# Optimization experiments

Measured on AMD Instinct MI355X. Metric: run time of the kernel, lower is better.

Reference implementation:

```python
import jax, jax.numpy as jnp
import numpy as np

B, L, H, NH, DH = 2, 4096, 768, 12, 64
W_ = 128          # one-sided sliding window
NL = 2            # encoder layers
VOCAB, OUT, FF = 50265, 384, 3072
EPS = 1e-5


def _ln(x, s, b):
    m = jnp.mean(x, axis=-1, keepdims=True)
    v = jnp.mean((x - m) ** 2, axis=-1, keepdims=True)
    return (x - m) / jnp.sqrt(v + EPS) * s + b


def _attn(x, amask, Wq, bq, Wk, bk, Wv, bv, Wo, bo):
    # x: [B,L,H]; sliding-window attention (one-sided W_) + global token 0
    def heads(Wt, bt):
        return (x @ Wt + bt).reshape(B, L, NH, DH).transpose(0, 2, 1, 3)  # [B,NH,L,DH]
    q, k, v = heads(Wq, bq), heads(Wk, bk), heads(Wv, bv)
    scale = 1.0 / np.sqrt(DH).astype(np.float32)
    C = W_
    nC = L // C
    qc = q.reshape(B, NH, nC, C, DH)

    def blocks(t):  # gather [prev, self, next] key chunks -> [B,NH,nC,3C,DH]
        tc = t.reshape(B, NH, nC, C, DH)
        tp = jnp.pad(tc, ((0, 0), (0, 0), (1, 1), (0, 0), (0, 0)))
        return jnp.concatenate([tp[:, :, :-2], tp[:, :, 1:-1], tp[:, :, 2:]], axis=3)

    k3, v3 = blocks(k), blocks(v)
    s_loc = jnp.einsum('bhncd,bhnkd->bhnck', qc, k3) * scale  # [B,NH,nC,C,3C]

    pos_k = (jnp.arange(nC)[:, None] - 1) * C + jnp.arange(3 * C)[None, :]  # [nC,3C]
    pos_q = jnp.arange(nC)[:, None] * C + jnp.arange(C)[None, :]            # [nC,C]
    within = jnp.abs(pos_q[:, :, None] - pos_k[:, None, :]) <= W_           # [nC,C,3C]
    valid = (pos_k >= 0) & (pos_k < L) & (pos_k != 0)  # key 0 handled as global column
    mk = amask[:, jnp.clip(pos_k, 0, L - 1)] > 0        # [B,nC,3C]
    m = within[None, None] & valid[None, None, :, None, :] & mk[:, None, :, None, :]
    s_loc = jnp.where(m, s_loc, -1e9)

    # every token also attends to the global token 0
    s_g = jnp.einsum('bhld,bhd->bhl', q, k[:, :, 0]) * scale  # [B,NH,L]
    s = jnp.concatenate([s_loc.reshape(B, NH, L, 3 * C), s_g[..., None]], axis=-1)
    p = jax.nn.softmax(s, axis=-1)
    p_loc = p[..., :3 * C].reshape(B, NH, nC, C, 3 * C)
    out = jnp.einsum('bhnck,bhnkd->bhncd', p_loc, v3).reshape(B, NH, L, DH)
    out = out + p[..., -1:] * v[:, :, 0][:, :, None, :]

    # global token 0 attends to everything
    s0 = jnp.einsum('bhd,bhld->bhl', q[:, :, 0], k) * scale
    s0 = jnp.where(amask[:, None, :] > 0, s0, -1e9)
    o0 = jnp.einsum('bhl,bhld->bhd', jax.nn.softmax(s0, axis=-1), v)
    out = out.at[:, :, 0, :].set(o0)

    out = out.transpose(0, 2, 1, 3).reshape(B, L, H)
    return out @ Wo + bo


def setup_inputs() -> dict:
    key = jax.random.key(0)
    ks = jax.random.split(key, 16)
    p = lambda k_, sh: 0.02 * jax.random.normal(k_, sh, jnp.float32)
    return {
        'input_ids': jax.random.randint(ks[0], (B, L), 0, VOCAB, dtype=jnp.int32),
        'attention_mask': jnp.ones((B, L), jnp.int32),
        'word_emb': p(ks[1], (VOCAB, H)),
        'pos_emb': p(ks[2], (L, H)),
        'emb_ln_s': jnp.ones((H,), jnp.float32), 'emb_ln_b': jnp.zeros((H,), jnp.float32),
        'Wq': p(ks[3], (NL, H, H)), 'bq': jnp.zeros((NL, H), jnp.float32),
        'Wk': p(ks[4], (NL, H, H)), 'bk': jnp.zeros((NL, H), jnp.float32),
        'Wv': p(ks[5], (NL, H, H)), 'bv': jnp.zeros((NL, H), jnp.float32),
        'Wo': p(ks[6], (NL, H, H)), 'bo': jnp.zeros((NL, H), jnp.float32),
        'ln1_s': jnp.ones((NL, H), jnp.float32), 'ln1_b': jnp.zeros((NL, H), jnp.float32),
        'W1': p(ks[7], (NL, H, FF)), 'b1': jnp.zeros((NL, FF), jnp.float32),
        'W2': p(ks[8], (NL, FF, H)), 'b2': jnp.zeros((NL, H), jnp.float32),
        'ln2_s': jnp.ones((NL, H), jnp.float32), 'ln2_b': jnp.zeros((NL, H), jnp.float32),
        'Wfc': p(ks[9], (H, OUT)), 'bfc': jnp.zeros((OUT,), jnp.float32),
    }


def reference(input_ids, attention_mask, word_emb, pos_emb, emb_ln_s, emb_ln_b,
              Wq, bq, Wk, bk, Wv, bv, Wo, bo, ln1_s, ln1_b,
              W1, b1, W2, b2, ln2_s, ln2_b, Wfc, bfc):
    x = word_emb[input_ids] + pos_emb[None]
    x = _ln(x, emb_ln_s, emb_ln_b)
    for l in range(NL):
        a = _attn(x, attention_mask, Wq[l], bq[l], Wk[l], bk[l], Wv[l], bv[l], Wo[l], bo[l])
        x = _ln(x + a, ln1_s[l], ln1_b[l])
        h = jax.nn.gelu(x @ W1[l] + b1[l])
        x = _ln(x + h @ W2[l] + b2[l], ln2_s[l], ln2_b[l])
    v_dn = x @ Wfc + bfc           # [B,L,OUT]
    cls = v_dn[:, 0]               # fc(last_hidden[:,0]) == v_dn[:,0]
    return v_dn, cls
```

## Files before the change

kernel.cpp:

```cpp
#include <hip/hip_runtime.h>
#include <hip/hip_bf16.h>
#include <stdint.h>

#define L_SEQ 4096
#define H_DIM 768
#define N_HEADS 12
#define D_HEAD 64
#define N_CHUNK 32
#define CHUNK 128
#define FF_DIM 3072
#define OUT_DIM 384
#define BATCH 2
#define EPS_LN 1e-5f
#define M_ROWS (BATCH * L_SEQ)
#define QKV_LD (3 * H_DIM)
#define NSEG 16

typedef unsigned short u16;
typedef __bf16 bx8 __attribute__((ext_vector_type(8)));
typedef float fx4 __attribute__((ext_vector_type(4)));
typedef u16 ux8 __attribute__((ext_vector_type(8)));

__device__ __forceinline__ u16 f2bf(float f) {
  union { float f; unsigned u; } x; x.f = f;
  unsigned r = x.u + 0x7fffu + ((x.u >> 16) & 1u);
  return (u16)(r >> 16);
}
__device__ __forceinline__ float bf2f(u16 v) {
  union { unsigned u; float f; } x; x.u = ((unsigned)v) << 16;
  return x.f;
}

__device__ __forceinline__ void gload16(const void* g, void* l) {
  __builtin_amdgcn_global_load_lds((const __attribute__((address_space(1))) void*)g,
                                   (__attribute__((address_space(3))) void*)l, 16, 0, 0);
}

template<int OUT_BF16, int DO_GELU>
__global__ __launch_bounds__(256, 3)
void gemm_s(const u16* __restrict__ A, const u16* __restrict__ Bt,
            const float* __restrict__ bias,
            float* __restrict__ Cf, u16* __restrict__ Cb,
            int N, int K)
{
  __shared__ __align__(16) u16 As[128 * 64];
  __shared__ __align__(16) u16 Bs[128 * 64];
  const int tid = threadIdx.x;
  const int lane = tid & 63, w = tid >> 6;
  const int c16 = lane & 15, g = lane >> 4;
  const int wr = w >> 1, wc = w & 1;

  const int nbn = N >> 7;
  int id = blockIdx.x;
  id = (id & 7) * (gridDim.x >> 3) + (id >> 3);
  const int bm = id / nbn, bn = id % nbn;

  const int srow = w * 8 + (lane >> 3);
  const int schunk = (lane & 7) ^ (lane >> 3);
  const u16* sA = A + (size_t)(bm * 128 + srow) * K + schunk * 8;
  const u16* sB = Bt + (size_t)(bn * 128 + srow) * K + schunk * 8;
  const int wdst = w * 512;

  fx4 acc[4][4] = {};

  for (int k0 = 0; k0 < K; k0 += 64) {
    #pragma unroll
    for (int i = 0; i < 4; i++) {
      gload16(sA + (size_t)(i * 32) * K + k0, &As[i * 2048 + wdst]);
      gload16(sB + (size_t)(i * 32) * K + k0, &Bs[i * 2048 + wdst]);
    }
    __syncthreads();
    #pragma unroll
    for (int h = 0; h < 2; h++) {
      bx8 af[4], bf[4];
      #pragma unroll
      for (int m = 0; m < 4; m++) {
        const int row = wr * 64 + m * 16 + c16;
        af[m] = *(const bx8*)&As[row * 64 + (((h << 2) + g) ^ (c16 & 7)) * 8];
      }
      #pragma unroll
      for (int n = 0; n < 4; n++) {
        const int row = wc * 64 + n * 16 + c16;
        bf[n] = *(const bx8*)&Bs[row * 64 + (((h << 2) + g) ^ (c16 & 7)) * 8];
      }
      #pragma unroll
      for (int m = 0; m < 4; m++)
        #pragma unroll
        for (int n = 0; n < 4; n++)
          acc[m][n] = __builtin_amdgcn_mfma_f32_16x16x32_bf16(af[m], bf[n], acc[m][n], 0, 0, 0);
    }
    __syncthreads();
  }

  const int row0 = bm * 128 + wr * 64 + g * 4;
  const int col0 = bn * 128 + wc * 64 + c16;
  #pragma unroll
  for (int n = 0; n < 4; n++) {
    const int col = col0 + n * 16;
    const float bb = bias[col];
    #pragma unroll
    for (int m = 0; m < 4; m++) {
      #pragma unroll
      for (int r = 0; r < 4; r++) {
        float y = acc[m][n][r] + bb;
        if (DO_GELU) {
          const float tt = y;
          y = 0.5f * tt * (1.0f + tanhf(0.7978845608f * (tt + 0.044715f * tt * tt * tt)));
        }
        const size_t idx = (size_t)(row0 + m * 16 + r) * N + col;
        if (OUT_BF16) Cb[idx] = f2bf(y);
        else Cf[idx] = y;
      }
    }
  }
}

#define V_STR 424

__global__ __launch_bounds__(512, 2)
void attn_local_kernel(const u16* __restrict__ qkv, const int* __restrict__ amask,
                       u16* __restrict__ attnout)
{
  __shared__ __align__(16) u16 Vlds[64 * V_STR];
  __shared__ __align__(16) u16 Plds[8 * 16 * V_STR];

  const int tid = threadIdx.x;
  const int lane = tid & 63, w = tid >> 6;
  const int c16 = lane & 15, g = lane >> 4;

  const int bh = blockIdx.x >> 5;
  const int n = blockIdx.x & 31;
  const int b = bh / N_HEADS, h = bh % N_HEADS;

  const u16* qkvb = qkv + (size_t)b * L_SEQ * QKV_LD + h * D_HEAD;
  const int chunk_lo = n * CHUNK - CHUNK;

  for (int idx = tid; idx < 416 * 8; idx += 512) {
    const int j = idx >> 3, d8 = (idx & 7) * 8;
    if (j >= 385) {
      #pragma unroll
      for (int i = 0; i < 8; i++) Vlds[(d8 + i) * V_STR + j] = 0;
    } else {
      int pos = (j == 384) ? 0 : chunk_lo + j;
      if (pos < 0 || pos >= L_SEQ) pos = 0;
      ux8 vv = *(const ux8*)(qkvb + (size_t)pos * QKV_LD + 2 * H_DIM + d8);
      #pragma unroll
      for (int i = 0; i < 8; i++) Vlds[(d8 + i) * V_STR + j] = vv[i];
    }
  }

  const int qrow = n * CHUNK + w * 16 + c16;
  const u16* qp = qkvb + (size_t)qrow * QKV_LD + g * 8;
  const bx8 aq0 = *(const bx8*)qp;
  const bx8 aq1 = *(const bx8*)(qp + 32);

  unsigned kvm = 0;
  #pragma unroll
  for (int kf = 0; kf < 24; kf++) {
    const int pos = chunk_lo + kf * 16 + c16;
    bool ok = (pos >= 1) && (pos < L_SEQ);
    if (ok) ok = (amask[b * L_SEQ + pos] > 0);
    kvm |= ((unsigned)ok) << kf;
  }

  fx4 s[26];
  #pragma unroll
  for (int kf = 0; kf < 25; kf++) {
    int pos = (kf == 24) ? 0 : chunk_lo + kf * 16 + c16;
    if (pos < 0 || pos >= L_SEQ) pos = 0;
    const u16* kp = qkvb + (size_t)pos * QKV_LD + H_DIM + g * 8;
    const bx8 b0 = *(const bx8*)kp;
    const bx8 b1 = *(const bx8*)(kp + 32);
    fx4 a = {};
    a = __builtin_amdgcn_mfma_f32_16x16x32_bf16(aq0, b0, a, 0, 0, 0);
    a = __builtin_amdgcn_mfma_f32_16x16x32_bf16(aq1, b1, a, 0, 0, 0);
    s[kf] = a;
  }

  const int cq = w * 16 + g * 4;
  float mx[4], sm[4];
  #pragma unroll
  for (int r = 0; r < 4; r++) mx[r] = -3.0e38f;
  #pragma unroll
  for (int kf = 0; kf < 25; kf++) {
    const int j = kf * 16 + c16;
    const bool kv = (kf < 24) ? (((kvm >> kf) & 1u) != 0) : (c16 == 0);
    #pragma unroll
    for (int r = 0; r < 4; r++) {
      const int c = cq + r;
      const bool keep = kv && (kf == 24 || (j >= c && j <= c + 256));
      const float val = keep ? s[kf][r] * 0.125f : -1.0e9f;
      s[kf][r] = val;
      mx[r] = fmaxf(mx[r], val);
    }
  }
  #pragma unroll
  for (int r = 0; r < 4; r++) {
    float m = mx[r];
    m = fmaxf(m, __shfl_xor(m, 1));
    m = fmaxf(m, __shfl_xor(m, 2));
    m = fmaxf(m, __shfl_xor(m, 4));
    m = fmaxf(m, __shfl_xor(m, 8));
    mx[r] = m;
    sm[r] = 0.f;
  }
  #pragma unroll
  for (int kf = 0; kf < 25; kf++)
    #pragma unroll
    for (int r = 0; r < 4; r++) {
      const float p = __expf(s[kf][r] - mx[r]);
      s[kf][r] = p;
      sm[r] += p;
    }
  float rinv[4];
  #pragma unroll
  for (int r = 0; r < 4; r++) {
    float t = sm[r];
    t += __shfl_xor(t, 1);
    t += __shfl_xor(t, 2);
    t += __shfl_xor(t, 4);
    t += __shfl_xor(t, 8);
    rinv[r] = 1.0f / t;
  }
  s[25] = (fx4){0.f, 0.f, 0.f, 0.f};

  u16* pb = Plds + (size_t)w * 16 * V_STR;
  #pragma unroll
  for (int kf = 0; kf < 26; kf++) {
    const int j = kf * 16 + c16;
    #pragma unroll
    for (int r = 0; r < 4; r++)
      pb[(g * 4 + r) * V_STR + j] = f2bf(s[kf][r]);
  }
  __syncthreads();

  fx4 o[4] = {};
  const u16* pr = Plds + (size_t)(w * 16 + c16) * V_STR + g * 8;
  #pragma unroll
  for (int kt = 0; kt < 13; kt++) {
    const bx8 pa = *(const bx8*)(pr + kt * 32);
    #pragma unroll
    for (int df = 0; df < 4; df++) {
      const bx8 vvf = *(const bx8*)&Vlds[(df * 16 + c16) * V_STR + kt * 32 + g * 8];
      o[df] = __builtin_amdgcn_mfma_f32_16x16x32_bf16(pa, vvf, o[df], 0, 0, 0);
    }
  }

  u16* ob = attnout + (size_t)b * L_SEQ * H_DIM + h * D_HEAD;
  const int posq = n * CHUNK + w * 16 + g * 4;
  #pragma unroll
  for (int df = 0; df < 4; df++)
    #pragma unroll
    for (int r = 0; r < 4; r++)
      ob[(size_t)(posq + r) * H_DIM + df * 16 + c16] = f2bf(o[df][r] * rinv[r]);
}

__global__ __launch_bounds__(256)
void attn_g_score(const u16* __restrict__ qkv, const int* __restrict__ amask,
                  float* __restrict__ sbuf, float* __restrict__ pmax)
{
  __shared__ float qs[D_HEAD];
  __shared__ float red[4];
  const int seg = blockIdx.x, bh = blockIdx.y;
  const int b = bh / N_HEADS, h = bh % N_HEADS;
  const u16* base = qkv + (size_t)b * L_SEQ * QKV_LD + h * D_HEAD;
  const int tid = threadIdx.x;

  if (tid < D_HEAD) qs[tid] = bf2f(base[tid]);
  __syncthreads();

  const int l = seg * 256 + tid;
  const ux8* kp = (const ux8*)(base + (size_t)l * QKV_LD + H_DIM);
  float dot = 0.f;
  #pragma unroll
  for (int i = 0; i < 8; i++) {
    const ux8 kv = kp[i];
    #pragma unroll
    for (int j = 0; j < 8; j++) dot += qs[i * 8 + j] * bf2f(kv[j]);
  }
  float sv = dot * 0.125f;
  if (amask[b * L_SEQ + l] == 0) sv = -1.0e9f;
  sbuf[(size_t)bh * L_SEQ + l] = sv;

  float m = sv;
  #pragma unroll
  for (int off = 32; off > 0; off >>= 1) m = fmaxf(m, __shfl_xor(m, off));
  if ((tid & 63) == 0) red[tid >> 6] = m;
  __syncthreads();
  if (tid == 0)
    pmax[bh * NSEG + seg] = fmaxf(fmaxf(red[0], red[1]), fmaxf(red[2], red[3]));
}

__global__ __launch_bounds__(256)
void attn_g_pv(const u16* __restrict__ qkv, const float* __restrict__ sbuf,
               const float* __restrict__ pmax, float* __restrict__ psum,
               float* __restrict__ po)
{
  __shared__ float es[256];
  __shared__ float red[4];
  const int seg = blockIdx.x, bh = blockIdx.y;
  const int b = bh / N_HEADS, h = bh % N_HEADS;
  const int tid = threadIdx.x;

  float M = -3.0e38f;
  #pragma unroll
  for (int i = 0; i < NSEG; i++) M = fmaxf(M, pmax[bh * NSEG + i]);

  const int l = seg * 256 + tid;
  const float e = __expf(sbuf[(size_t)bh * L_SEQ + l] - M);
  es[tid] = e;

  float t = e;
  #pragma unroll
  for (int off = 32; off > 0; off >>= 1) t += __shfl_xor(t, off);
  if ((tid & 63) == 0) red[tid >> 6] = t;
  __syncthreads();
  if (tid == 0) psum[bh * NSEG + seg] = red[0] + red[1] + red[2] + red[3];

  const int d = tid & 63, grp = tid >> 6;
  const u16* vb = qkv + (size_t)b * L_SEQ * QKV_LD + h * D_HEAD + 2 * H_DIM + d;
  float acc = 0.f;
  #pragma unroll 4
  for (int i = 0; i < 64; i++) {
    const int ll = seg * 256 + grp * 64 + i;
    acc += es[grp * 64 + i] * bf2f(vb[(size_t)ll * QKV_LD]);
  }
  po[(((size_t)bh * NSEG + seg) * 4 + grp) * D_HEAD + d] = acc;
}

__global__ __launch_bounds__(64)
void attn_g_combine(const float* __restrict__ psum, const float* __restrict__ po,
                    u16* __restrict__ attnout)
{
  const int bh = blockIdx.x;
  const int b = bh / N_HEADS, h = bh % N_HEADS;
  const int d = threadIdx.x;
  float S = 0.f;
  #pragma unroll
  for (int i = 0; i < NSEG; i++) S += psum[bh * NSEG + i];
  float acc = 0.f;
  #pragma unroll
  for (int i = 0; i < NSEG * 4; i++)
    acc += po[((size_t)bh * NSEG * 4 + i) * D_HEAD + d];
  attnout[(size_t)b * L_SEQ * H_DIM + h * D_HEAD + d] = f2bf(acc / S);
}

__device__ __forceinline__ void block_stats(float sum, float sq, float* red,
                                            float& mean, float& rstd)
{
  const int lane = threadIdx.x & 63, wv = threadIdx.x >> 6;
  #pragma unroll
  for (int off = 32; off > 0; off >>= 1) {
    sum += __shfl_xor(sum, off);
    sq  += __shfl_xor(sq, off);
  }
  if (lane == 0) { red[wv] = sum; red[4 + wv] = sq; }
  __syncthreads();
  sum = red[0] + red[1] + red[2] + red[3];
  sq  = red[4] + red[5] + red[6] + red[7];
  mean = sum * (1.0f / H_DIM);
  const float var = sq * (1.0f / H_DIM) - mean * mean;
  rstd = rsqrtf(var + EPS_LN);
}

__global__ __launch_bounds__(256)
void embed_ln_kernel(const int* __restrict__ ids, const float* __restrict__ wemb,
                     const float* __restrict__ pemb, const float* __restrict__ gam,
                     const float* __restrict__ bet, float* __restrict__ xf,
                     u16* __restrict__ xb)
{
  __shared__ float red[8];
  const int row = blockIdx.x, tid = threadIdx.x;
  const int l = row & (L_SEQ - 1);
  const int id = ids[row];
  float v[3]; float sum = 0.f, sq = 0.f;
  #pragma unroll
  for (int i = 0; i < 3; i++) {
    const int c = tid + i * 256;
    const float t = wemb[(size_t)id * H_DIM + c] + pemb[(size_t)l * H_DIM + c];
    v[i] = t; sum += t; sq += t * t;
  }
  float mean, rstd;
  block_stats(sum, sq, red, mean, rstd);
  #pragma unroll
  for (int i = 0; i < 3; i++) {
    const int c = tid + i * 256;
    const float y = (v[i] - mean) * rstd * gam[c] + bet[c];
    xf[(size_t)row * H_DIM + c] = y;
    xb[(size_t)row * H_DIM + c] = f2bf(y);
  }
}

__global__ __launch_bounds__(256)
void add_ln_kernel(float* xio, const float* __restrict__ yin,
                   const float* __restrict__ gam, const float* __restrict__ bet,
                   u16* __restrict__ xb)
{
  __shared__ float red[8];
  const int row = blockIdx.x, tid = threadIdx.x;
  float v[3]; float sum = 0.f, sq = 0.f;
  #pragma unroll
  for (int i = 0; i < 3; i++) {
    const int c = tid + i * 256;
    const float t = xio[(size_t)row * H_DIM + c] + yin[(size_t)row * H_DIM + c];
    v[i] = t; sum += t; sq += t * t;
  }
  float mean, rstd;
  block_stats(sum, sq, red, mean, rstd);
  #pragma unroll
  for (int i = 0; i < 3; i++) {
    const int c = tid + i * 256;
    const float y = (v[i] - mean) * rstd * gam[c] + bet[c];
    xio[(size_t)row * H_DIM + c] = y;
    xb[(size_t)row * H_DIM + c] = f2bf(y);
  }
}

__global__ __launch_bounds__(256)
void transpose_w_kernel(const float* __restrict__ W, u16* __restrict__ Wt, int K, int N)
{
  __shared__ float tile[32][33];
  const int k0 = blockIdx.x * 32, n0 = blockIdx.y * 32;
  const int tx = threadIdx.x & 31, ty = threadIdx.x >> 5;
  #pragma unroll
  for (int i = 0; i < 32; i += 8)
    tile[ty + i][tx] = W[(size_t)(k0 + ty + i) * N + n0 + tx];
  __syncthreads();
  #pragma unroll
  for (int i = 0; i < 32; i += 8)
    Wt[(size_t)(n0 + ty + i) * K + k0 + tx] = f2bf(tile[tx][ty + i]);
}

__global__ void concat3_kernel(const float* __restrict__ a, const float* __restrict__ b,
                               const float* __restrict__ c, float* __restrict__ out)
{
  const int i = blockIdx.x * 256 + threadIdx.x;
  if (i < H_DIM) out[i] = a[i];
  else if (i < 2 * H_DIM) out[i] = b[i - H_DIM];
  else if (i < 3 * H_DIM) out[i] = c[i - 2 * H_DIM];
}

__global__ void cls_copy_kernel(const float* __restrict__ vdn, float* __restrict__ cls)
{
  const int i = blockIdx.x * 256 + threadIdx.x;
  if (i < BATCH * OUT_DIM)
    cls[i] = vdn[(size_t)(i / OUT_DIM) * L_SEQ * OUT_DIM + (i % OUT_DIM)];
}

extern "C" void kernel_launch(void* const* d_in, const int* in_sizes, int n_in,
                              void* d_out, int out_size, void* d_ws, size_t ws_size,
                              hipStream_t stream)
{
  (void)in_sizes; (void)n_in; (void)out_size; (void)ws_size;
  const int*   ids   = (const int*)d_in[0];
  const int*   amask = (const int*)d_in[1];
  const float* wemb  = (const float*)d_in[2];
  const float* pemb  = (const float*)d_in[3];
  const float* elns  = (const float*)d_in[4];
  const float* elnb  = (const float*)d_in[5];
  const float* Wq    = (const float*)d_in[6];
  const float* bq    = (const float*)d_in[7];
  const float* Wk    = (const float*)d_in[8];
  const float* bk    = (const float*)d_in[9];
  const float* Wv    = (const float*)d_in[10];
  const float* bv    = (const float*)d_in[11];
  const float* Wo    = (const float*)d_in[12];
  const float* bo    = (const float*)d_in[13];
  const float* ln1s  = (const float*)d_in[14];
  const float* ln1b  = (const float*)d_in[15];
  const float* W1    = (const float*)d_in[16];
  const float* b1    = (const float*)d_in[17];
  const float* W2    = (const float*)d_in[18];
  const float* b2    = (const float*)d_in[19];
  const float* ln2s  = (const float*)d_in[20];
  const float* ln2b  = (const float*)d_in[21];
  const float* Wfc   = (const float*)d_in[22];
  const float* bfc   = (const float*)d_in[23];

  char* ws = (char*)d_ws;
  size_t off = 0;
  auto alloc = [&](size_t bytes) -> void* {
    void* p = ws + off;
    off += (bytes + 255) & ~(size_t)255;
    return p;
  };
  float* xf   = (float*)alloc((size_t)M_ROWS * H_DIM * 4);
  float* proj = (float*)alloc((size_t)M_ROWS * H_DIM * 4);
  u16* xb     = (u16*)alloc((size_t)M_ROWS * H_DIM * 2);
  u16* big    = (u16*)alloc((size_t)M_ROWS * FF_DIM * 2);
  u16* attno  = (u16*)alloc((size_t)M_ROWS * H_DIM * 2);
  u16* wqkvT  = (u16*)alloc((size_t)QKV_LD * H_DIM * 2);
  u16* woT    = (u16*)alloc((size_t)H_DIM * H_DIM * 2);
  u16* w1T    = (u16*)alloc((size_t)FF_DIM * H_DIM * 2);
  u16* w2T    = (u16*)alloc((size_t)H_DIM * FF_DIM * 2);
  u16* wfcT   = (u16*)alloc((size_t)OUT_DIM * H_DIM * 2);
  float* bqkv = (float*)alloc(QKV_LD * 4);
  float* gsc  = (float*)alloc((size_t)BATCH * N_HEADS * L_SEQ * 4);
  float* gpm  = (float*)alloc((size_t)BATCH * N_HEADS * NSEG * 4);
  float* gps  = (float*)alloc((size_t)BATCH * N_HEADS * NSEG * 4);
  float* gpo  = (float*)alloc((size_t)BATCH * N_HEADS * NSEG * 4 * D_HEAD * 4);

  u16* qkvb = big;
  u16* ff1  = big;

  embed_ln_kernel<<<M_ROWS, 256, 0, stream>>>(ids, wemb, pemb, elns, elnb, xf, xb);

  for (int l = 0; l < 2; l++) {
    const size_t wof = (size_t)l * H_DIM * H_DIM;
    transpose_w_kernel<<<dim3(24, 24), 256, 0, stream>>>(Wq + wof, wqkvT, H_DIM, H_DIM);
    transpose_w_kernel<<<dim3(24, 24), 256, 0, stream>>>(Wk + wof, wqkvT + (size_t)H_DIM * H_DIM, H_DIM, H_DIM);
    transpose_w_kernel<<<dim3(24, 24), 256, 0, stream>>>(Wv + wof, wqkvT + (size_t)2 * H_DIM * H_DIM, H_DIM, H_DIM);
    transpose_w_kernel<<<dim3(24, 24), 256, 0, stream>>>(Wo + wof, woT, H_DIM, H_DIM);
    transpose_w_kernel<<<dim3(24, 96), 256, 0, stream>>>(W1 + (size_t)l * H_DIM * FF_DIM, w1T, H_DIM, FF_DIM);
    transpose_w_kernel<<<dim3(96, 24), 256, 0, stream>>>(W2 + (size_t)l * FF_DIM * H_DIM, w2T, FF_DIM, H_DIM);
    concat3_kernel<<<9, 256, 0, stream>>>(bq + l * H_DIM, bk + l * H_DIM, bv + l * H_DIM, bqkv);

    gemm_s<1, 0><<<(M_ROWS / 128) * (QKV_LD / 128), 256, 0, stream>>>(
        xb, wqkvT, bqkv, nullptr, qkvb, QKV_LD, H_DIM);
    attn_local_kernel<<<BATCH * N_HEADS * N_CHUNK, 512, 0, stream>>>(qkvb, amask, attno);
    attn_g_score<<<dim3(NSEG, BATCH * N_HEADS), 256, 0, stream>>>(qkvb, amask, gsc, gpm);
    attn_g_pv<<<dim3(NSEG, BATCH * N_HEADS), 256, 0, stream>>>(qkvb, gsc, gpm, gps, gpo);
    attn_g_combine<<<BATCH * N_HEADS, 64, 0, stream>>>(gps, gpo, attno);
    gemm_s<0, 0><<<(M_ROWS / 128) * (H_DIM / 128), 256, 0, stream>>>(
        attno, woT, bo + l * H_DIM, proj, nullptr, H_DIM, H_DIM);
    add_ln_kernel<<<M_ROWS, 256, 0, stream>>>(xf, proj, ln1s + l * H_DIM, ln1b + l * H_DIM, xb);
    gemm_s<1, 1><<<(M_ROWS / 128) * (FF_DIM / 128), 256, 0, stream>>>(
        xb, w1T, b1 + l * FF_DIM, nullptr, ff1, FF_DIM, H_DIM);
    gemm_s<0, 0><<<(M_ROWS / 128) * (H_DIM / 128), 256, 0, stream>>>(
        ff1, w2T, b2 + l * H_DIM, proj, nullptr, H_DIM, FF_DIM);
    add_ln_kernel<<<M_ROWS, 256, 0, stream>>>(xf, proj, ln2s + l * H_DIM, ln2b + l * H_DIM, xb);
  }

  transpose_w_kernel<<<dim3(24, 12), 256, 0, stream>>>(Wfc, wfcT, H_DIM, OUT_DIM);
  float* vdn = (float*)d_out;
  gemm_s<0, 0><<<(M_ROWS / 128) * (OUT_DIM / 128), 256, 0, stream>>>(
      xb, wfcT, bfc, vdn, nullptr, OUT_DIM, H_DIM);
  cls_copy_kernel<<<3, 256, 0, stream>>>(vdn, vdn + (size_t)BATCH * L_SEQ * OUT_DIM);
}
```

Baseline: 675.1 us.

## Use 128x256 eight-wave GEMM tiles and bf16 projection outputs

```diff
diff --git a/kernel.cpp b/kernel.cpp
--- a/kernel.cpp
+++ b/kernel.cpp
@@ -37,50 +37,48 @@
 }
 
 template<int OUT_BF16, int DO_GELU>
-__global__ __launch_bounds__(256, 3)
-void gemm_s(const u16* __restrict__ A, const u16* __restrict__ Bt,
+__global__ __launch_bounds__(512, 4)
+void gemm_w(const u16* __restrict__ A, const u16* __restrict__ Bt,
             const float* __restrict__ bias,
             float* __restrict__ Cf, u16* __restrict__ Cb,
             int N, int K)
 {
   __shared__ __align__(16) u16 As[128 * 64];
-  __shared__ __align__(16) u16 Bs[128 * 64];
+  __shared__ __align__(16) u16 Bs[256 * 64];
   const int tid = threadIdx.x;
   const int lane = tid & 63, w = tid >> 6;
   const int c16 = lane & 15, g = lane >> 4;
-  const int wr = w >> 1, wc = w & 1;
-
-  const int nbn = N >> 7;
+  const int wm = w >> 2, wn = w & 3;
+
+  const int nbn = N >> 8;
   int id = blockIdx.x;
   id = (id & 7) * (gridDim.x >> 3) + (id >> 3);
   const int bm = id / nbn, bn = id % nbn;
 
-  const int srow = w * 8 + (lane >> 3);
-  const int schunk = (lane & 7) ^ (lane >> 3);
-  const u16* sA = A + (size_t)(bm * 128 + srow) * K + schunk * 8;
-  const u16* sB = Bt + (size_t)(bn * 128 + srow) * K + schunk * 8;
-  const int wdst = w * 512;
+  const int schunk = (lane & 7) ^ ((lane >> 3) & 7);
+  const u16* sA = A + (size_t)(bm * 128 + w * 16 + (lane >> 3)) * K + schunk * 8;
+  const u16* sB = Bt + (size_t)(bn * 256 + w * 32 + (lane >> 3)) * K + schunk * 8;
 
   fx4 acc[4][4] = {};
 
   for (int k0 = 0; k0 < K; k0 += 64) {
-    #pragma unroll
-    for (int i = 0; i < 4; i++) {
-      gload16(sA + (size_t)(i * 32) * K + k0, &As[i * 2048 + wdst]);
-      gload16(sB + (size_t)(i * 32) * K + k0, &Bs[i * 2048 + wdst]);
-    }
+    gload16(sA + k0, &As[w * 1024]);
+    gload16(sA + (size_t)8 * K + k0, &As[w * 1024 + 512]);
+    #pragma unroll
+    for (int i = 0; i < 4; i++)
+      gload16(sB + (size_t)(i * 8) * K + k0, &Bs[w * 2048 + i * 512]);
     __syncthreads();
     #pragma unroll
     for (int h = 0; h < 2; h++) {
       bx8 af[4], bf[4];
       #pragma unroll
       for (int m = 0; m < 4; m++) {
-        const int row = wr * 64 + m * 16 + c16;
+        const int row = wm * 64 + m * 16 + c16;
         af[m] = *(const bx8*)&As[row * 64 + (((h << 2) + g) ^ (c16 & 7)) * 8];
       }
       #pragma unroll
       for (int n = 0; n < 4; n++) {
-        const int row = wc * 64 + n * 16 + c16;
+        const int row = wn * 64 + n * 16 + c16;
         bf[n] = *(const bx8*)&Bs[row * 64 + (((h << 2) + g) ^ (c16 & 7)) * 8];
       }
       #pragma unroll
@@ -92,8 +90,8 @@
     __syncthreads();
   }
 
-  const int row0 = bm * 128 + wr * 64 + g * 4;
-  const int col0 = bn * 128 + wc * 64 + c16;
+  const int row0 = bm * 128 + wm * 64 + g * 4;
+  const int col0 = bn * 256 + wn * 64 + c16;
   #pragma unroll
   for (int n = 0; n < 4; n++) {
     const int col = col0 + n * 16;
@@ -115,6 +113,85 @@
   }
 }
 
+template<int OUT_BF16, int DO_GELU>
+__global__ __launch_bounds__(256, 3)
+void gemm_s(const u16* __restrict__ A, const u16* __restrict__ Bt,
+            const float* __restrict__ bias,
+            float* __restrict__ Cf, u16* __restrict__ Cb,
+            int N, int K)
+{
+  __shared__ __align__(16) u16 As[128 * 64];
+  __shared__ __align__(16) u16 Bs[128 * 64];
+  const int tid = threadIdx.x;
+  const int lane = tid & 63, w = tid >> 6;
+  const int c16 = lane & 15, g = lane >> 4;
+  const int wr = w >> 1, wc = w & 1;
+
+  const int nbn = N >> 7;
+  int id = blockIdx.x;
+  id = (id & 7) * (gridDim.x >> 3) + (id >> 3);
+  const int bm = id / nbn, bn = id % nbn;
+
+  const int srow = w * 8 + (lane >> 3);
+  const int schunk = (lane & 7) ^ (lane >> 3);
+  const u16* sA = A + (size_t)(bm * 128 + srow) * K + schunk * 8;
+  const u16* sB = Bt + (size_t)(bn * 128 + srow) * K + schunk * 8;
+  const int wdst = w * 512;
+
+  fx4 acc[4][4] = {};
+
+  for (int k0 = 0; k0 < K; k0 += 64) {
+    #pragma unroll
+    for (int i = 0; i < 4; i++) {
+      gload16(sA + (size_t)(i * 32) * K + k0, &As[i * 2048 + wdst]);
+      gload16(sB + (size_t)(i * 32) * K + k0, &Bs[i * 2048 + wdst]);
+    }
+    __syncthreads();
+    #pragma unroll
+    for (int h = 0; h < 2; h++) {
+      bx8 af[4], bf[4];
+      #pragma unroll
+      for (int m = 0; m < 4; m++) {
+        const int row = wr * 64 + m * 16 + c16;
+        af[m] = *(const bx8*)&As[row * 64 + (((h << 2) + g) ^ (c16 & 7)) * 8];
+      }
+      #pragma unroll
+      for (int n = 0; n < 4; n++) {
+        const int row = wc * 64 + n * 16 + c16;
+        bf[n] = *(const bx8*)&Bs[row * 64 + (((h << 2) + g) ^ (c16 & 7)) * 8];
+      }
+      #pragma unroll
+      for (int m = 0; m < 4; m++)
+        #pragma unroll
+        for (int n = 0; n < 4; n++)
+          acc[m][n] = __builtin_amdgcn_mfma_f32_16x16x32_bf16(af[m], bf[n], acc[m][n], 0, 0, 0);
+    }
+    __syncthreads();
+  }
+
+  const int row0 = bm * 128 + wr * 64 + g * 4;
+  const int col0 = bn * 128 + wc * 64 + c16;
+  #pragma unroll
+  for (int n = 0; n < 4; n++) {
+    const int col = col0 + n * 16;
+    const float bb = bias[col];
+    #pragma unroll
+    for (int m = 0; m < 4; m++) {
+      #pragma unroll
+      for (int r = 0; r < 4; r++) {
+        float y = acc[m][n][r] + bb;
+        if (DO_GELU) {
+          const float tt = y;
+          y = 0.5f * tt * (1.0f + tanhf(0.7978845608f * (tt + 0.044715f * tt * tt * tt)));
+        }
+        const size_t idx = (size_t)(row0 + m * 16 + r) * N + col;
+        if (OUT_BF16) Cb[idx] = f2bf(y);
+        else Cf[idx] = y;
+      }
+    }
+  }
+}
+
 #define V_STR 424
 
 __global__ __launch_bounds__(512, 2)
@@ -392,7 +469,7 @@
 }
 
 __global__ __launch_bounds__(256)
-void add_ln_kernel(float* xio, const float* __restrict__ yin,
+void add_ln_kernel(float* xio, const u16* __restrict__ yin,
                    const float* __restrict__ gam, const float* __restrict__ bet,
                    u16* __restrict__ xb)
 {
@@ -402,7 +479,7 @@
   #pragma unroll
   for (int i = 0; i < 3; i++) {
     const int c = tid + i * 256;
-    const float t = xio[(size_t)row * H_DIM + c] + yin[(size_t)row * H_DIM + c];
+    const float t = xio[(size_t)row * H_DIM + c] + bf2f(yin[(size_t)row * H_DIM + c]);
     v[i] = t; sum += t; sq += t * t;
   }
   float mean, rstd;
@@ -485,7 +562,7 @@
     return p;
   };
   float* xf   = (float*)alloc((size_t)M_ROWS * H_DIM * 4);
-  float* proj = (float*)alloc((size_t)M_ROWS * H_DIM * 4);
+  u16* projb  = (u16*)alloc((size_t)M_ROWS * H_DIM * 2);
   u16* xb     = (u16*)alloc((size_t)M_ROWS * H_DIM * 2);
   u16* big    = (u16*)alloc((size_t)M_ROWS * FF_DIM * 2);
   u16* attno  = (u16*)alloc((size_t)M_ROWS * H_DIM * 2);
@@ -515,20 +592,20 @@
     transpose_w_kernel<<<dim3(96, 24), 256, 0, stream>>>(W2 + (size_t)l * FF_DIM * H_DIM, w2T, FF_DIM, H_DIM);
     concat3_kernel<<<9, 256, 0, stream>>>(bq + l * H_DIM, bk + l * H_DIM, bv + l * H_DIM, bqkv);
 
-    gemm_s<1, 0><<<(M_ROWS / 128) * (QKV_LD / 128), 256, 0, stream>>>(
+    gemm_w<1, 0><<<(M_ROWS / 128) * (QKV_LD / 256), 512, 0, stream>>>(
         xb, wqkvT, bqkv, nullptr, qkvb, QKV_LD, H_DIM);
     attn_local_kernel<<<BATCH * N_HEADS * N_CHUNK, 512, 0, stream>>>(qkvb, amask, attno);
     attn_g_score<<<dim3(NSEG, BATCH * N_HEADS), 256, 0, stream>>>(qkvb, amask, gsc, gpm);
     attn_g_pv<<<dim3(NSEG, BATCH * N_HEADS), 256, 0, stream>>>(qkvb, gsc, gpm, gps, gpo);
     attn_g_combine<<<BATCH * N_HEADS, 64, 0, stream>>>(gps, gpo, attno);
-    gemm_s<0, 0><<<(M_ROWS / 128) * (H_DIM / 128), 256, 0, stream>>>(
-        attno, woT, bo + l * H_DIM, proj, nullptr, H_DIM, H_DIM);
-    add_ln_kernel<<<M_ROWS, 256, 0, stream>>>(xf, proj, ln1s + l * H_DIM, ln1b + l * H_DIM, xb);
-    gemm_s<1, 1><<<(M_ROWS / 128) * (FF_DIM / 128), 256, 0, stream>>>(
+    gemm_w<1, 0><<<(M_ROWS / 128) * (H_DIM / 256), 512, 0, stream>>>(
+        attno, woT, bo + l * H_DIM, nullptr, projb, H_DIM, H_DIM);
+    add_ln_kernel<<<M_ROWS, 256, 0, stream>>>(xf, projb, ln1s + l * H_DIM, ln1b + l * H_DIM, xb);
+    gemm_w<1, 1><<<(M_ROWS / 128) * (FF_DIM / 256), 512, 0, stream>>>(
         xb, w1T, b1 + l * FF_DIM, nullptr, ff1, FF_DIM, H_DIM);
-    gemm_s<0, 0><<<(M_ROWS / 128) * (H_DIM / 128), 256, 0, stream>>>(
-        ff1, w2T, b2 + l * H_DIM, proj, nullptr, H_DIM, FF_DIM);
-    add_ln_kernel<<<M_ROWS, 256, 0, stream>>>(xf, proj, ln2s + l * H_DIM, ln2b + l * H_DIM, xb);
+    gemm_w<1, 0><<<(M_ROWS / 128) * (H_DIM / 256), 512, 0, stream>>>(
+        ff1, w2T, b2 + l * H_DIM, nullptr, projb, H_DIM, FF_DIM);
+    add_ln_kernel<<<M_ROWS, 256, 0, stream>>>(xf, projb, ln2s + l * H_DIM, ln2b + l * H_DIM, xb);
   }
 
   transpose_w_kernel<<<dim3(24, 12), 256, 0, stream>>>(Wfc, wfcT, H_DIM, OUT_DIM);
```

Measured after the change: 710.8 us. +5.3%, slower.
